# Kernel tuning notes

Hardware: AMD Instinct MI355X
Metric: run time of the kernel (lower is better)

The kernel has to match this reference:

```python
import jax, jax.numpy as jnp
import numpy as np

N_HEADS = 16
D_MODEL = 1024
SEQ = 1024
WIDTH = 32
BATCH = 4


def _make_graph(n, w, seed=0):
    # Mirrors sparse_attention_graph: normal offsets around each node index,
    # mod n, then per-row duplicates are replaced by global-ish tokens 0,1,...
    rng = np.random.default_rng(seed)
    pulls = rng.normal(0.0, float(w), size=(n, w)).astype(np.int64)
    adj = (pulls + np.arange(n)[:, None]) % n
    rows = []
    for r in adj:
        u = np.unique(r)
        i = 0
        while u.shape[0] < w:
            d = w - u.shape[0]
            u = np.unique(np.concatenate([np.arange(i, i + d), u]))
            i += d
        rows.append(np.sort(u))
    return jnp.asarray(np.stack(rows), dtype=jnp.int32)


def setup_inputs() -> dict:
    key = jax.random.key(0)
    ks = jax.random.split(key, 5)
    scale = 1.0 / np.sqrt(D_MODEL).astype(np.float32)
    return {
        "hidden_states": jax.random.normal(ks[0], (BATCH, SEQ, D_MODEL), jnp.float32),
        "wq_kernel": jax.random.normal(ks[1], (D_MODEL, D_MODEL), jnp.float32) * scale,
        "wq_bias": jnp.zeros((D_MODEL,), jnp.float32),
        "wk_kernel": jax.random.normal(ks[2], (D_MODEL, D_MODEL), jnp.float32) * scale,
        "wk_bias": jnp.zeros((D_MODEL,), jnp.float32),
        "wv_kernel": jax.random.normal(ks[3], (D_MODEL, D_MODEL), jnp.float32) * scale,
        "wv_bias": jnp.zeros((D_MODEL,), jnp.float32),
        "wo_kernel": jax.random.normal(ks[4], (D_MODEL, D_MODEL), jnp.float32) * scale,
        "wo_bias": jnp.zeros((D_MODEL,), jnp.float32),
        "graph": _make_graph(SEQ, WIDTH),
    }


def reference(hidden_states, wq_kernel, wq_bias, wk_kernel, wk_bias,
              wv_kernel, wv_bias, wo_kernel, wo_bias, graph):
    B, N, D = hidden_states.shape
    H = N_HEADS
    depth = D // H

    def split_heads(x):
        return x.reshape(B, N, H, depth).transpose(0, 2, 1, 3)  # [B,H,N,depth]

    q = split_heads(hidden_states @ wq_kernel + wq_bias)
    k = split_heads(hidden_states @ wk_kernel + wk_bias)
    v = split_heads(hidden_states @ wv_kernel + wv_bias)

    # Gather neighbor keys per node: [B,H,N,W,depth]; dot only on graph edges.
    kg = k[:, :, graph, :]
    dots = jnp.einsum('bhnd,bhnwd->bhnw', q, kg)

    # Scatter edge dots into dense [B,H,N,N] score matrix; non-edges stay 0,
    # exactly as dot_circle_product does (softmax then runs over the FULL row).
    rows = jnp.arange(N)[:, None]  # broadcasts with graph [N,W]
    scores = jnp.zeros((B, H, N, N), hidden_states.dtype).at[:, :, rows, graph].set(dots)

    attn = jax.nn.softmax(scores / jnp.sqrt(jnp.asarray(depth, scores.dtype)), axis=-1)
    out = jnp.einsum('bhij,bhjd->bhid', attn, v)          # [B,H,N,depth]
    out = out.transpose(0, 2, 1, 3).reshape(B, N, D)      # merge heads
    output = out @ wo_kernel + wo_bias
    return (output, attn)
```

## Files before the change

### kernel.cpp

```cpp
#include <hip/hip_runtime.h>
#include <hip/hip_bf16.h>

constexpr int B = 4;
constexpr int N = 1024;
constexpr int D = 1024;
constexpr int H = 16;
constexpr int DEPTH = 64;
constexpr int W = 32;
constexpr int LDQKV = 3072;
constexpr int SROWS = 10240;

typedef _Float16 f16x8 __attribute__((ext_vector_type(8)));
typedef float f32x4 __attribute__((ext_vector_type(4)));
typedef unsigned short us8 __attribute__((ext_vector_type(8)));
typedef unsigned short us4 __attribute__((ext_vector_type(4)));

__device__ __forceinline__ float h2f(unsigned short u) {
  return (float)__builtin_bit_cast(_Float16, u);
}

__device__ __forceinline__ void load_lds16(const void* g, void* l) {
  unsigned int lo = (unsigned int)(unsigned long long)l;
  __builtin_amdgcn_global_load_lds(
      (const __attribute__((address_space(1))) unsigned int*)g,
      (__attribute__((address_space(3))) unsigned int*)lo, 16, 0, 0);
}

__global__ __launch_bounds__(256) void prep_all(
    const float* __restrict__ hidden, const float* __restrict__ wq,
    const float* __restrict__ wk, const float* __restrict__ wv,
    const float* __restrict__ wo, const float* __restrict__ bq,
    const float* __restrict__ bk, const float* __restrict__ bv,
    unsigned short* __restrict__ A16, unsigned short* __restrict__ BTh,
    unsigned short* __restrict__ WoTh, float* __restrict__ biasq) {
  __shared__ float sf[64][65];
  const int t = threadIdx.x;
  int blk = blockIdx.x;

  if (blk < 2048) {
    const size_t i = ((size_t)blk * 256 + t) * 8;
    float4 a = *(const float4*)(hidden + i);
    float4 b = *(const float4*)(hidden + i + 4);
    float xs[8] = {a.x, a.y, a.z, a.w, b.x, b.y, b.z, b.w};
    us8 hv;
#pragma unroll
    for (int j = 0; j < 8; j++)
      hv[j] = __builtin_bit_cast(unsigned short, (_Float16)xs[j]);
    *(us8*)(A16 + i) = hv;
    return;
  }
  blk -= 2048;
  if (blk < 1024) {
    const int which = blk >> 8;
    const int sub = blk & 255;
    const float* w = which == 0 ? wq : which == 1 ? wk : which == 2 ? wv : wo;
    unsigned short* oh = which < 3 ? BTh : WoTh;
    const int rowOff = which < 3 ? which * 1024 : 0;

    const int tn = (sub & 15) * 64;
    const int tk = (sub >> 4) * 64;
#pragma unroll
    for (int i = 0; i < 4; i++) {
      int f = i * 256 + t;
      int r = f >> 4, c4 = (f & 15) * 4;
      float4 v = *(const float4*)(w + (size_t)(tk + r) * 1024 + tn + c4);
      sf[r][c4 + 0] = v.x; sf[r][c4 + 1] = v.y;
      sf[r][c4 + 2] = v.z; sf[r][c4 + 3] = v.w;
    }
    __syncthreads();
    const int n = t >> 2;
    const int kc = (t & 3) * 16;
    us8 hv[2];
#pragma unroll
    for (int half = 0; half < 2; half++) {
#pragma unroll
      for (int j = 0; j < 8; j++) {
        float x = sf[kc + half * 8 + j][n];
        hv[half][j] = __builtin_bit_cast(unsigned short, (_Float16)x);
      }
    }
    size_t dst = (size_t)(rowOff + tn + n) * 1024 + tk + kc;
    *(us8*)(oh + dst) = hv[0];
    *(us8*)(oh + dst + 8) = hv[1];
    return;
  }
  blk -= 1024;
  int i = blk * 256 + t;
  biasq[i] = i < 1024 ? bq[i] : (i < 2048 ? bk[i - 1024] : bv[i - 2048]);
}

__global__ __launch_bounds__(256, 2) void gemm_qkv(
    const unsigned short* __restrict__ A16, const unsigned short* __restrict__ BTh,
    const float* __restrict__ bias, unsigned short* __restrict__ Cout,
    float* __restrict__ vpart, int K, int Nn) {
  __shared__ __align__(16) unsigned short sA[2 * 128 * 32];
  __shared__ __align__(16) unsigned short sB[2 * 256 * 32];
  __shared__ float vred[2][2][8][16];

  const int tid = threadIdx.x;
  const int lane = tid & 63;
  const int wave = tid >> 6;
  const int wr = wave >> 1, wc = wave & 1;

  const int gx = gridDim.x;
  const int nwg = gx * gridDim.y;
  int bid = blockIdx.y * gx + blockIdx.x;
  bid = (bid & 7) * (nwg >> 3) + (bid >> 3);
  const int bm = (bid / gx) * 128;
  const int bn = (bid % gx) * 256;

  size_t aoff[2];
  int ldsA[2];
#pragma unroll
  for (int c = 0; c < 2; c++) {
    const int chunk = wave + 4 * c;
    const int e = chunk * 512 + lane * 8;
    const int r = e >> 5;
    const int kpos = (e >> 3) & 3;
    const int ksrc = kpos ^ ((r >> 1) & 3);
    aoff[c] = (size_t)(bm + r) * K + ksrc * 8;
    ldsA[c] = chunk * 512;
  }
  size_t boff[4];
  int ldsB[4];
#pragma unroll
  for (int c = 0; c < 4; c++) {
    const int chunk = wave + 4 * c;
    const int e = chunk * 512 + lane * 8;
    const int r = e >> 5;
    const int kpos = (e >> 3) & 3;
    const int ksrc = kpos ^ ((r >> 1) & 3);
    boff[c] = (size_t)(bn + r) * K + ksrc * 8;
    ldsB[c] = chunk * 512;
  }

  const int fr = lane & 15;
  const int fkg = lane >> 4;

  int aroff[4], broff[8];
#pragma unroll
  for (int m = 0; m < 4; m++) {
    const int ra = wr * 64 + m * 16 + fr;
    aroff[m] = ra * 32 + ((fkg ^ ((ra >> 1) & 3)) << 3);
  }
#pragma unroll
  for (int n = 0; n < 8; n++) {
    const int rb = wc * 128 + n * 16 + fr;
    broff[n] = rb * 32 + ((fkg ^ ((rb >> 1) & 3)) << 3);
  }

  f32x4 acc[4][8] = {};

  const int NT = K >> 5;
#pragma unroll
  for (int c = 0; c < 2; c++) load_lds16(A16 + aoff[c], sA + ldsA[c]);
#pragma unroll
  for (int c = 0; c < 4; c++) load_lds16(BTh + boff[c], sB + ldsB[c]);
  __syncthreads();

  int cur = 0;
  for (int t = 0; t < NT; t++) {
    const int boA = cur * (128 * 32);
    const int boB = cur * (256 * 32);
    const int nxA = (cur ^ 1) * (128 * 32);
    const int nxB = (cur ^ 1) * (256 * 32);
    if (t + 1 < NT) {
      const int k0 = (t + 1) << 5;
#pragma unroll
      for (int c = 0; c < 2; c++) load_lds16(A16 + aoff[c] + k0, sA + nxA + ldsA[c]);
#pragma unroll
      for (int c = 0; c < 4; c++) load_lds16(BTh + boff[c] + k0, sB + nxB + ldsB[c]);
    }
    f16x8 a[4], bh[8];
#pragma unroll
    for (int m = 0; m < 4; m++) a[m] = *(const f16x8*)(sA + boA + aroff[m]);
#pragma unroll
    for (int n = 0; n < 8; n++) bh[n] = *(const f16x8*)(sB + boB + broff[n]);
    __builtin_amdgcn_s_setprio(1);
#pragma unroll
    for (int m = 0; m < 4; m++)
#pragma unroll
      for (int n = 0; n < 8; n++)
        acc[m][n] = __builtin_amdgcn_mfma_f32_16x16x32_f16(a[m], bh[n], acc[m][n], 0, 0, 0);
    __builtin_amdgcn_s_setprio(0);
    __syncthreads();
    cur ^= 1;
  }

#pragma unroll
  for (int m = 0; m < 4; m++) {
    const int row = bm + wr * 64 + m * 16 + fkg * 4;
#pragma unroll
    for (int n = 0; n < 8; n++) {
      const int col = bn + wc * 128 + n * 16 + fr;
      const float bsv = bias[col];
#pragma unroll
      for (int j = 0; j < 4; j++) {
        const float v = acc[m][n][j] + bsv;
        Cout[(size_t)(row + j) * Nn + col] =
            __builtin_bit_cast(unsigned short, (_Float16)v);
      }
    }
  }

  if (bn >= 2048) {
    float csum[8];
#pragma unroll
    for (int n = 0; n < 8; n++) {
      float s = 0.f;
#pragma unroll
      for (int m = 0; m < 4; m++)
#pragma unroll
        for (int j = 0; j < 4; j++) s += acc[m][n][j];
      s += __shfl_xor(s, 16);
      s += __shfl_xor(s, 32);
      csum[n] = s;
    }
    if (fkg == 0) {
#pragma unroll
      for (int n = 0; n < 8; n++) vred[wr][wc][n][fr] = csum[n];
    }
    __syncthreads();
    if (wr == 0 && fkg == 0) {
#pragma unroll
      for (int n = 0; n < 8; n++) {
        const int d = bn - 2048 + wc * 128 + n * 16 + fr;
        vpart[(size_t)(bm >> 7) * 1024 + d] = csum[n] + vred[1][wc][n][fr];
      }
    }
  }
}

__global__ __launch_bounds__(256, 4) void gemm_o(
    const unsigned short* __restrict__ A16, const unsigned short* __restrict__ BTh,
    const float* __restrict__ bias, float* __restrict__ Cout, int K, int Nn) {
  __shared__ __align__(16) unsigned short sA[2 * 128 * 32];
  __shared__ __align__(16) unsigned short sB[2 * 128 * 32];

  const int tid = threadIdx.x;
  const int lane = tid & 63;
  const int wave = tid >> 6;
  const int wr = wave >> 1, wc = wave & 1;

  const int gx = gridDim.x;
  const int nwg = gx * gridDim.y;
  int bid = blockIdx.y * gx + blockIdx.x;
  bid = (bid & 7) * (nwg >> 3) + (bid >> 3);
  const int bm = (bid / gx) * 128;
  const int bn = (bid % gx) * 128;

  size_t aoff[2], boff[2];
  int ldsoff[2];
#pragma unroll
  for (int c = 0; c < 2; c++) {
    const int chunk = wave + 4 * c;
    const int e = chunk * 512 + lane * 8;
    const int r = e >> 5;
    const int kpos = (e >> 3) & 3;
    const int ksrc = kpos ^ ((r >> 1) & 3);
    aoff[c] = (size_t)(bm + r) * K + ksrc * 8;
    boff[c] = (size_t)(bn + r) * K + ksrc * 8;
    ldsoff[c] = chunk * 512;
  }

  const int fr = lane & 15;
  const int fkg = lane >> 4;

  int aroff[4], broff[4];
#pragma unroll
  for (int m = 0; m < 4; m++) {
    const int ra = wr * 64 + m * 16 + fr;
    aroff[m] = ra * 32 + ((fkg ^ ((ra >> 1) & 3)) << 3);
    const int rb = wc * 64 + m * 16 + fr;
    broff[m] = rb * 32 + ((fkg ^ ((rb >> 1) & 3)) << 3);
  }

  f32x4 acc[4][4] = {};

  const int NT = K >> 5;
#pragma unroll
  for (int c = 0; c < 2; c++) {
    load_lds16(A16 + aoff[c], sA + ldsoff[c]);
    load_lds16(BTh + boff[c], sB + ldsoff[c]);
  }
  __syncthreads();

  int cur = 0;
  for (int t = 0; t < NT; t++) {
    const int bo_ = cur * (128 * 32);
    const int nx_ = (cur ^ 1) * (128 * 32);
    if (t + 1 < NT) {
      const int k0 = (t + 1) << 5;
#pragma unroll
      for (int c = 0; c < 2; c++) {
        load_lds16(A16 + aoff[c] + k0, sA + nx_ + ldsoff[c]);
        load_lds16(BTh + boff[c] + k0, sB + nx_ + ldsoff[c]);
      }
    }
    f16x8 a[4], bh[4];
#pragma unroll
    for (int m = 0; m < 4; m++) a[m] = *(const f16x8*)(sA + bo_ + aroff[m]);
#pragma unroll
    for (int n = 0; n < 4; n++) bh[n] = *(const f16x8*)(sB + bo_ + broff[n]);
    __builtin_amdgcn_s_setprio(1);
#pragma unroll
    for (int m = 0; m < 4; m++)
#pragma unroll
      for (int n = 0; n < 4; n++)
        acc[m][n] = __builtin_amdgcn_mfma_f32_16x16x32_f16(a[m], bh[n], acc[m][n], 0, 0, 0);
    __builtin_amdgcn_s_setprio(0);
    __syncthreads();
    cur ^= 1;
  }

#pragma unroll
  for (int m = 0; m < 4; m++) {
    const int row = bm + wr * 64 + m * 16 + fkg * 4;
#pragma unroll
    for (int n = 0; n < 4; n++) {
      const int col = bn + wc * 64 + n * 16 + fr;
      const float bsv = bias[col];
#pragma unroll
      for (int j = 0; j < 4; j++)
        Cout[(size_t)(row + j) * Nn + col] = acc[m][n][j] + bsv;
    }
  }
}

__global__ __launch_bounds__(256) void vsum_comb(const float* __restrict__ vpart,
                                                 const float* __restrict__ biasq,
                                                 float* __restrict__ vsum) {
  const int i = blockIdx.x * 256 + threadIdx.x;
  const int b = i >> 10, d = i & 1023;
  float s = 1024.0f * biasq[2048 + d];
#pragma unroll
  for (int c = 0; c < 8; c++) s += vpart[(size_t)(b * 8 + c) * 1024 + d];
  vsum[i] = s;
}

__global__ __launch_bounds__(256) void attn_pass1(
    const unsigned short* __restrict__ qkv16, const float* __restrict__ vsum,
    const int* __restrict__ graph, float* __restrict__ pbuf,
    float* __restrict__ basebuf, unsigned short* __restrict__ O16,
    float* __restrict__ attn) {
  const int blk = blockIdx.x;
  const int n = blk & (N - 1);
  const int hg = (blk >> 10) & 3;
  const int b = blk >> 12;
  const int wave = threadIdx.x >> 6;
  const int lane = threadIdx.x & 63;
  const int h = hg * 4 + wave;
  const int bid = (b * H + h) * N + n;

  __shared__ float q_sh[4][DEPTH];
  __shared__ int g_sh[W];
  __shared__ float p_sh[4][W];
  __shared__ float rowbuf[4][N];

  const unsigned short* qrow = qkv16 + (size_t)(b * N + n) * LDQKV + h * DEPTH;
  q_sh[wave][lane] = h2f(qrow[lane]);
  if (threadIdx.x < W) g_sh[threadIdx.x] = graph[n * W + threadIdx.x];
  __syncthreads();

  const int w = lane >> 1;
  const int half = lane & 1;
  const unsigned short* krow =
      qkv16 + 1024 + (size_t)(b * N + g_sh[w]) * LDQKV + h * DEPTH + half * 32;
  float acc = 0.f;
#pragma unroll
  for (int j8 = 0; j8 < 4; j8++) {
    us8 kv = *(const us8*)(krow + j8 * 8);
    const float* qh = &q_sh[wave][half * 32 + j8 * 8];
#pragma unroll
    for (int e = 0; e < 8; e++) acc += h2f(kv[e]) * qh[e];
  }
  acc += __shfl_xor(acc, 1);
  const float dot = acc * 0.125f;

  float m = dot;
#pragma unroll
  for (int off = 2; off < 64; off <<= 1) m = fmaxf(m, __shfl_xor(m, off));
  m = fmaxf(m, 0.f);

  const float e = expf(dot - m);
  float s = e;
#pragma unroll
  for (int off = 1; off < 64; off <<= 1) s += __shfl_xor(s, off);
  s *= 0.5f;

  const float em = expf(-m);
  const float Z = (float)(N - W) * em + s;
  const float inv = 1.f / Z;
  const float base = em * inv;
  const float pw = e * inv;

  if (half == 0) p_sh[wave][w] = pw;
  __syncthreads();

  const bool fused = (bid >= SROWS);
  if (!fused) {
    if (half == 0) pbuf[(size_t)bid * W + w] = pw;
    if (lane == 0) basebuf[bid] = base;
  }

  const unsigned short* vbase = qkv16 + 2048;
  const int col = h * DEPTH + lane;
  float ov = base * vsum[b * D + col];
#pragma unroll 4
  for (int ww = 0; ww < W; ww++) {
    ov += (p_sh[wave][ww] - base) *
          h2f(vbase[(size_t)(b * N + g_sh[ww]) * LDQKV + col]);
  }
  _Float16 hh = (_Float16)ov;
  O16[(size_t)(b * N + n) * D + col] = __builtin_bit_cast(unsigned short, hh);

  f32x4* rw = (f32x4*)rowbuf[wave];
  f32x4 b4v = {base, base, base, base};
#pragma unroll
  for (int i = 0; i < 4; i++) rw[lane + 64 * i] = b4v;
  __syncthreads();
  if (fused && half == 0) rowbuf[wave][g_sh[w]] = pw;
  __syncthreads();
  if (fused) {
    f32x4* dst = (f32x4*)(attn + (size_t)bid * N);
#pragma unroll
    for (int i = 0; i < 4; i++)
      __builtin_nontemporal_store(rw[lane + 64 * i], dst + lane + 64 * i);
  }
}

__global__ __launch_bounds__(256) void attn_fill_rem(
    const float* __restrict__ pbuf, const float* __restrict__ basebuf,
    const int* __restrict__ graph, float* __restrict__ attn) {
  const int blk = blockIdx.x;
  const int n = blk & (N - 1);
  const int hh = blk >> 10;
  const int t = threadIdx.x;

  __shared__ float row[2][N];
  __shared__ int g_sh[W];

  const int bid0 = hh * N + n;
  const int bid1 = (hh + 5) * N + n;

  if (t < W) g_sh[t] = graph[n * W + t];
  const float base0 = basebuf[bid0];
  const float base1 = basebuf[bid1];
  f32x4* row40 = (f32x4*)row[0];
  f32x4* row41 = (f32x4*)row[1];
  row40[t] = (f32x4){base0, base0, base0, base0};
  row41[t] = (f32x4){base1, base1, base1, base1};
  __syncthreads();
  if (t < 2 * W) {
    const int r = t >> 5;
    const int w = t & 31;
    const int bidr = r == 0 ? bid0 : bid1;
    row[r][g_sh[w]] = pbuf[(size_t)bidr * W + w];
  }
  __syncthreads();
  __builtin_nontemporal_store(row40[t], (f32x4*)(attn + (size_t)bid0 * N) + t);
  __builtin_nontemporal_store(row41[t], (f32x4*)(attn + (size_t)bid1 * N) + t);
}

extern "C" void kernel_launch(void* const* d_in, const int* in_sizes, int n_in,
                              void* d_out, int out_size, void* d_ws, size_t ws_size,
                              hipStream_t stream) {
  const float* hidden = (const float*)d_in[0];
  const float* wq = (const float*)d_in[1];
  const float* bq = (const float*)d_in[2];
  const float* wk = (const float*)d_in[3];
  const float* bk = (const float*)d_in[4];
  const float* wv = (const float*)d_in[5];
  const float* bv = (const float*)d_in[6];
  const float* wo = (const float*)d_in[7];
  const float* bo = (const float*)d_in[8];
  const int* graph = (const int*)d_in[9];

  float* out0 = (float*)d_out;
  float* attnp = out0 + (size_t)B * N * D;

  const size_t M1 = (size_t)1024 * 1024;
  unsigned short* qkv16 = (unsigned short*)attnp;
  unsigned short* A16 = (unsigned short*)(attnp + 6 * M1);
  unsigned short* O16 = A16;
  unsigned short* BTh = (unsigned short*)(attnp + 8 * M1);
  unsigned short* WoTh = (unsigned short*)(attnp + 9 * M1 + 524288);

  float* pbuf = (float*)d_ws;
  float* basebuf = pbuf + (size_t)B * H * N * W;
  float* vsumb = basebuf + (size_t)B * H * N;
  float* biasq = pbuf;
  float* vpart = pbuf + 4096;

  prep_all<<<3084, 256, 0, stream>>>(hidden, wq, wk, wv, wo, bq, bk, bv,
                                     A16, BTh, WoTh, biasq);

  gemm_qkv<<<dim3(12, 32), 256, 0, stream>>>(A16, BTh, biasq, qkv16, vpart,
                                             1024, 3072);

  vsum_comb<<<16, 256, 0, stream>>>(vpart, biasq, vsumb);

  attn_pass1<<<B * 4 * N, 256, 0, stream>>>(qkv16, vsumb, graph, pbuf, basebuf,
                                            O16, attnp);

  gemm_o<<<dim3(8, 32), 256, 0, stream>>>(O16, WoTh, bo, out0, 1024, 1024);

  attn_fill_rem<<<SROWS / 2, 256, 0, stream>>>(pbuf, basebuf, graph, attnp);
}
```

Measured before the change: 148.8 us.

## Fuse attention row fill into output GEMM launch to overlap with GEMM

Merges the output projection GEMM with the remaining attention-row fill work into one launch. The first 256 blocks run the GEMM and the next 6144 blocks each fill one attention row, so the memory-bound fill overlaps with the compute-bound GEMM. The fill rows that alias the workspace region holding WoTh and BTh are moved to a separate trailing kernel, and the WoTh/BTh placement is swapped so the fused fill does not overwrite WoTh while the GEMM still reads it. The fill also drops from two rows per block to one row per block, which raises block count and the per-row sync overhead.

```diff
diff --git a/kernel.cpp b/kernel.cpp
--- a/kernel.cpp
+++ b/kernel.cpp
@@ -8,7 +8,7 @@
 constexpr int DEPTH = 64;
 constexpr int W = 32;
 constexpr int LDQKV = 3072;
-constexpr int SROWS = 10240;
+constexpr int SROWS = 8704;
 
 typedef _Float16 f16x8 __attribute__((ext_vector_type(8)));
 typedef float f32x4 __attribute__((ext_vector_type(4)));
@@ -24,6 +24,20 @@
   __builtin_amdgcn_global_load_lds(
       (const __attribute__((address_space(1))) unsigned int*)g,
       (__attribute__((address_space(3))) unsigned int*)lo, 16, 0, 0);
+}
+
+__device__ __forceinline__ void fill_row(float* rowf, const float* pbuf,
+                                         const float* basebuf,
+                                         const int* graph, float* attn,
+                                         int row, int t) {
+  const int n = row & (N - 1);
+  const float base = basebuf[row];
+  f32x4* rw = (f32x4*)rowf;
+  rw[t] = (f32x4){base, base, base, base};
+  __syncthreads();
+  if (t < W) rowf[graph[n * W + t]] = pbuf[(size_t)row * W + t];
+  __syncthreads();
+  __builtin_nontemporal_store(rw[t], (f32x4*)(attn + (size_t)row * N) + t);
 }
 
 __global__ __launch_bounds__(256) void prep_all(
@@ -227,102 +241,6 @@
         const int d = bn - 2048 + wc * 128 + n * 16 + fr;
         vpart[(size_t)(bm >> 7) * 1024 + d] = csum[n] + vred[1][wc][n][fr];
       }
-    }
-  }
-}
-
-__global__ __launch_bounds__(256, 4) void gemm_o(
-    const unsigned short* __restrict__ A16, const unsigned short* __restrict__ BTh,
-    const float* __restrict__ bias, float* __restrict__ Cout, int K, int Nn) {
-  __shared__ __align__(16) unsigned short sA[2 * 128 * 32];
-  __shared__ __align__(16) unsigned short sB[2 * 128 * 32];
-
-  const int tid = threadIdx.x;
-  const int lane = tid & 63;
-  const int wave = tid >> 6;
-  const int wr = wave >> 1, wc = wave & 1;
-
-  const int gx = gridDim.x;
-  const int nwg = gx * gridDim.y;
-  int bid = blockIdx.y * gx + blockIdx.x;
-  bid = (bid & 7) * (nwg >> 3) + (bid >> 3);
-  const int bm = (bid / gx) * 128;
-  const int bn = (bid % gx) * 128;
-
-  size_t aoff[2], boff[2];
-  int ldsoff[2];
-#pragma unroll
-  for (int c = 0; c < 2; c++) {
-    const int chunk = wave + 4 * c;
-    const int e = chunk * 512 + lane * 8;
-    const int r = e >> 5;
-    const int kpos = (e >> 3) & 3;
-    const int ksrc = kpos ^ ((r >> 1) & 3);
-    aoff[c] = (size_t)(bm + r) * K + ksrc * 8;
-    boff[c] = (size_t)(bn + r) * K + ksrc * 8;
-    ldsoff[c] = chunk * 512;
-  }
-
-  const int fr = lane & 15;
-  const int fkg = lane >> 4;
-
-  int aroff[4], broff[4];
-#pragma unroll
-  for (int m = 0; m < 4; m++) {
-    const int ra = wr * 64 + m * 16 + fr;
-    aroff[m] = ra * 32 + ((fkg ^ ((ra >> 1) & 3)) << 3);
-    const int rb = wc * 64 + m * 16 + fr;
-    broff[m] = rb * 32 + ((fkg ^ ((rb >> 1) & 3)) << 3);
-  }
-
-  f32x4 acc[4][4] = {};
-
-  const int NT = K >> 5;
-#pragma unroll
-  for (int c = 0; c < 2; c++) {
-    load_lds16(A16 + aoff[c], sA + ldsoff[c]);
-    load_lds16(BTh + boff[c], sB + ldsoff[c]);
-  }
-  __syncthreads();
-
-  int cur = 0;
-  for (int t = 0; t < NT; t++) {
-    const int bo_ = cur * (128 * 32);
-    const int nx_ = (cur ^ 1) * (128 * 32);
-    if (t + 1 < NT) {
-      const int k0 = (t + 1) << 5;
-#pragma unroll
-      for (int c = 0; c < 2; c++) {
-        load_lds16(A16 + aoff[c] + k0, sA + nx_ + ldsoff[c]);
-        load_lds16(BTh + boff[c] + k0, sB + nx_ + ldsoff[c]);
-      }
-    }
-    f16x8 a[4], bh[4];
-#pragma unroll
-    for (int m = 0; m < 4; m++) a[m] = *(const f16x8*)(sA + bo_ + aroff[m]);
-#pragma unroll
-    for (int n = 0; n < 4; n++) bh[n] = *(const f16x8*)(sB + bo_ + broff[n]);
-    __builtin_amdgcn_s_setprio(1);
-#pragma unroll
-    for (int m = 0; m < 4; m++)
-#pragma unroll
-      for (int n = 0; n < 4; n++)
-        acc[m][n] = __builtin_amdgcn_mfma_f32_16x16x32_f16(a[m], bh[n], acc[m][n], 0, 0, 0);
-    __builtin_amdgcn_s_setprio(0);
-    __syncthreads();
-    cur ^= 1;
-  }
-
-#pragma unroll
-  for (int m = 0; m < 4; m++) {
-    const int row = bm + wr * 64 + m * 16 + fkg * 4;
-#pragma unroll
-    for (int n = 0; n < 4; n++) {
-      const int col = bn + wc * 64 + n * 16 + fr;
-      const float bsv = bias[col];
-#pragma unroll
-      for (int j = 0; j < 4; j++)
-        Cout[(size_t)(row + j) * Nn + col] = acc[m][n][j] + bsv;
     }
   }
 }
@@ -429,37 +347,113 @@
   }
 }
 
-__global__ __launch_bounds__(256) void attn_fill_rem(
+__global__ __launch_bounds__(256, 4) void gemm_o_fill(
+    const unsigned short* __restrict__ A16, const unsigned short* __restrict__ BTh,
+    const float* __restrict__ bias, float* __restrict__ Cout,
+    const float* __restrict__ pbuf, const float* __restrict__ basebuf,
+    const int* __restrict__ graph, float* __restrict__ attn, int K, int Nn) {
+  __shared__ __align__(16) unsigned short sA[2 * 128 * 32];
+  __shared__ __align__(16) unsigned short sB[2 * 128 * 32];
+
+  const int blk = blockIdx.x;
+  if (blk >= 256) {
+    fill_row((float*)sA, pbuf, basebuf, graph, attn, blk - 256, threadIdx.x);
+    return;
+  }
+
+  const int tid = threadIdx.x;
+  const int lane = tid & 63;
+  const int wave = tid >> 6;
+  const int wr = wave >> 1, wc = wave & 1;
+
+  int bid = blk;
+  bid = (bid & 7) * 32 + (bid >> 3);
+  const int bm = (bid >> 3) * 128;
+  const int bn = (bid & 7) * 128;
+
+  size_t aoff[2], boff[2];
+  int ldsoff[2];
+#pragma unroll
+  for (int c = 0; c < 2; c++) {
+    const int chunk = wave + 4 * c;
+    const int e = chunk * 512 + lane * 8;
+    const int r = e >> 5;
+    const int kpos = (e >> 3) & 3;
+    const int ksrc = kpos ^ ((r >> 1) & 3);
+    aoff[c] = (size_t)(bm + r) * K + ksrc * 8;
+    boff[c] = (size_t)(bn + r) * K + ksrc * 8;
+    ldsoff[c] = chunk * 512;
+  }
+
+  const int fr = lane & 15;
+  const int fkg = lane >> 4;
+
+  int aroff[4], broff[4];
+#pragma unroll
+  for (int m = 0; m < 4; m++) {
+    const int ra = wr * 64 + m * 16 + fr;
+    aroff[m] = ra * 32 + ((fkg ^ ((ra >> 1) & 3)) << 3);
+    const int rb = wc * 64 + m * 16 + fr;
+    broff[m] = rb * 32 + ((fkg ^ ((rb >> 1) & 3)) << 3);
+  }
+
+  f32x4 acc[4][4] = {};
+
+  const int NT = K >> 5;
+#pragma unroll
+  for (int c = 0; c < 2; c++) {
+    load_lds16(A16 + aoff[c], sA + ldsoff[c]);
+    load_lds16(BTh + boff[c], sB + ldsoff[c]);
+  }
+  __syncthreads();
+
+  int cur = 0;
+  for (int t = 0; t < NT; t++) {
+    const int bo_ = cur * (128 * 32);
+    const int nx_ = (cur ^ 1) * (128 * 32);
+    if (t + 1 < NT) {
+      const int k0 = (t + 1) << 5;
+#pragma unroll
+      for (int c = 0; c < 2; c++) {
+        load_lds16(A16 + aoff[c] + k0, sA + nx_ + ldsoff[c]);
+        load_lds16(BTh + boff[c] + k0, sB + nx_ + ldsoff[c]);
+      }
+    }
+    f16x8 a[4], bh[4];
+#pragma unroll
+    for (int m = 0; m < 4; m++) a[m] = *(const f16x8*)(sA + bo_ + aroff[m]);
+#pragma unroll
+    for (int n = 0; n < 4; n++) bh[n] = *(const f16x8*)(sB + bo_ + broff[n]);
+    __builtin_amdgcn_s_setprio(1);
+#pragma unroll
+    for (int m = 0; m < 4; m++)
+#pragma unroll
+      for (int n = 0; n < 4; n++)
+        acc[m][n] = __builtin_amdgcn_mfma_f32_16x16x32_f16(a[m], bh[n], acc[m][n], 0, 0, 0);
+    __builtin_amdgcn_s_setprio(0);
+    __syncthreads();
+    cur ^= 1;
+  }
+
+#pragma unroll
+  for (int m = 0; m < 4; m++) {
+    const int row = bm + wr * 64 + m * 16 + fkg * 4;
+#pragma unroll
+    for (int n = 0; n < 4; n++) {
+      const int col = bn + wc * 64 + n * 16 + fr;
+      const float bsv = bias[col];
+#pragma unroll
+      for (int j = 0; j < 4; j++)
+        Cout[(size_t)(row + j) * Nn + col] = acc[m][n][j] + bsv;
+    }
+  }
+}
+
+__global__ __launch_bounds__(256) void attn_fill_last(
     const float* __restrict__ pbuf, const float* __restrict__ basebuf,
     const int* __restrict__ graph, float* __restrict__ attn) {
-  const int blk = blockIdx.x;
-  const int n = blk & (N - 1);
-  const int hh = blk >> 10;
-  const int t = threadIdx.x;
-
-  __shared__ float row[2][N];
-  __shared__ int g_sh[W];
-
-  const int bid0 = hh * N + n;
-  const int bid1 = (hh + 5) * N + n;
-
-  if (t < W) g_sh[t] = graph[n * W + t];
-  const float base0 = basebuf[bid0];
-  const float base1 = basebuf[bid1];
-  f32x4* row40 = (f32x4*)row[0];
-  f32x4* row41 = (f32x4*)row[1];
-  row40[t] = (f32x4){base0, base0, base0, base0};
-  row41[t] = (f32x4){base1, base1, base1, base1};
-  __syncthreads();
-  if (t < 2 * W) {
-    const int r = t >> 5;
-    const int w = t & 31;
-    const int bidr = r == 0 ? bid0 : bid1;
-    row[r][g_sh[w]] = pbuf[(size_t)bidr * W + w];
-  }
-  __syncthreads();
-  __builtin_nontemporal_store(row40[t], (f32x4*)(attn + (size_t)bid0 * N) + t);
-  __builtin_nontemporal_store(row41[t], (f32x4*)(attn + (size_t)bid1 * N) + t);
+  __shared__ __align__(16) float rowf[N];
+  fill_row(rowf, pbuf, basebuf, graph, attn, 6144 + blockIdx.x, threadIdx.x);
 }
 
 extern "C" void kernel_launch(void* const* d_in, const int* in_sizes, int n_in,
@@ -483,8 +477,8 @@
   unsigned short* qkv16 = (unsigned short*)attnp;
   unsigned short* A16 = (unsigned short*)(attnp + 6 * M1);
   unsigned short* O16 = A16;
-  unsigned short* BTh = (unsigned short*)(attnp + 8 * M1);
-  unsigned short* WoTh = (unsigned short*)(attnp + 9 * M1 + 524288);
+  unsigned short* WoTh = (unsigned short*)(attnp + 8 * M1);
+  unsigned short* BTh = (unsigned short*)(attnp + 8 * M1 + 524288);
 
   float* pbuf = (float*)d_ws;
   float* basebuf = pbuf + (size_t)B * H * N * W;
@@ -503,7 +497,9 @@
   attn_pass1<<<B * 4 * N, 256, 0, stream>>>(qkv16, vsumb, graph, pbuf, basebuf,
                                             O16, attnp);
 
-  gemm_o<<<dim3(8, 32), 256, 0, stream>>>(O16, WoTh, bo, out0, 1024, 1024);
-
-  attn_fill_rem<<<SROWS / 2, 256, 0, stream>>>(pbuf, basebuf, graph, attnp);
-}
+  gemm_o_fill<<<256 + 6144, 256, 0, stream>>>(O16, WoTh, bo, out0, pbuf,
+                                              basebuf, graph, attnp,
+                                              1024, 1024);
+
+  attn_fill_last<<<8704 - 6144, 256, 0, stream>>>(pbuf, basebuf, graph, attnp);
+}
```

New measurement: 146.2 us. Within noise of the previous version (-1.8%).
